# Performance work log

Hardware: AMD Instinct MI355X
Metric: run time of the kernel (lower is better)

## Reference

```python
import jax, jax.numpy as jnp
import numpy as np

B, T, C = 4, 2048, 1024
N_HEAD = 16
HEAD = C // N_HEAD

def setup_inputs() -> dict:
    key = jax.random.key(0)
    ks = jax.random.split(key, 5)
    return {
        "x": jax.random.normal(ks[0], (B, T, C), dtype=jnp.float32),
        "W_attn": jax.random.normal(ks[1], (C, 3 * C), dtype=jnp.float32) * (C ** -0.5),
        "b_attn": jax.random.normal(ks[2], (3 * C,), dtype=jnp.float32) * 0.02,
        "W_proj": jax.random.normal(ks[3], (C, C), dtype=jnp.float32) * (C ** -0.5),
        "b_proj": jax.random.normal(ks[4], (C,), dtype=jnp.float32) * 0.02,
    }

def reference(x, W_attn, b_attn, W_proj, b_proj):
    Bx, Tx, Cx = x.shape
    qkv = x @ W_attn + b_attn  # [B,T,3C]
    q, k, v = jnp.split(qkv, 3, axis=2)
    # [B,T,H,D] -> [B,H,T,D]
    q = q.reshape(Bx, Tx, N_HEAD, HEAD).transpose(0, 2, 1, 3)
    k = k.reshape(Bx, Tx, N_HEAD, HEAD).transpose(0, 2, 1, 3)
    v = v.reshape(Bx, Tx, N_HEAD, HEAD).transpose(0, 2, 1, 3)
    att = jnp.einsum('bhqd,bhkd->bhqk', q, k) * (HEAD ** -0.5)
    causal = jnp.tril(jnp.ones((Tx, Tx), dtype=bool))
    att = jnp.where(causal, att, jnp.float32(-jnp.inf))
    att = jax.nn.softmax(att, axis=-1)
    y = jnp.einsum('bhqk,bhkd->bhqd', att, v)
    y = y.transpose(0, 2, 1, 3).reshape(Bx, Tx, Cx)
    return y @ W_proj + b_proj
```

## Files before the change

kernel.cpp:

```cpp
#include <hip/hip_runtime.h>
#include <stdint.h>

#define NB 4
#define TT 2048
#define CC 1024
#define NH 16
#define DD 64
#define BHH (NB*NH)
#define MROWS (NB*TT)

typedef uint16_t u16;
typedef uint32_t u32;
typedef __bf16 bf16x8 __attribute__((ext_vector_type(8)));
typedef float f32x4 __attribute__((ext_vector_type(4)));
typedef float f32x16 __attribute__((ext_vector_type(16)));

__device__ __forceinline__ u16 f2bf(float f) {
    union { float f; uint32_t u; } v; v.f = f;
    uint32_t u = v.u;
    return (u16)((u + 0x7FFF + ((u >> 16) & 1)) >> 16);
}

__device__ __forceinline__ u32 cvtpk(float lo, float hi) {
    u32 r;
    asm volatile("v_cvt_pk_bf16_f32 %0, %1, %2" : "=v"(r) : "v"(lo), "v"(hi));
    return r;
}

__device__ __forceinline__ void plswap(u32& a, u32& b) {
    asm volatile("v_permlane32_swap_b32 %0, %1" : "+v"(a), "+v"(b));
}

__device__ __forceinline__ bf16x8 mk8(u32 a, u32 b, u32 c, u32 d) {
    union { u32 u[4]; bf16x8 v; } x;
    x.u[0] = a; x.u[1] = b; x.u[2] = c; x.u[3] = d;
    return x.v;
}

__device__ __forceinline__ void gl_lds16(const u16* g, u16* l) {
    __builtin_amdgcn_global_load_lds(
        (const __attribute__((address_space(1))) unsigned int*)g,
        (__attribute__((address_space(3))) unsigned int*)l, 16, 0, 0);
}

__device__ __forceinline__ f32x4 mfma16(bf16x8 a, bf16x8 b, f32x4 c) {
    return __builtin_amdgcn_mfma_f32_16x16x32_bf16(a, b, c, 0, 0, 0);
}
__device__ __forceinline__ f32x16 mfma32(bf16x8 a, bf16x8 b, f32x16 c) {
    return __builtin_amdgcn_mfma_f32_32x32x16_bf16(a, b, c, 0, 0, 0);
}

__global__ __launch_bounds__(256) void k_f2b(const float* __restrict__ in,
                                             u16* __restrict__ out, int n) {
    const int i = (blockIdx.x * 256 + threadIdx.x) * 4;
    if (i >= n) return;
    const float4 v = *(const float4*)(in + i);
    ushort4 o;
    o.x = f2bf(v.x); o.y = f2bf(v.y); o.z = f2bf(v.z); o.w = f2bf(v.w);
    *(ushort4*)(out + i) = o;
}

__global__ __launch_bounds__(256) void k_transpose_cvt(const float* __restrict__ in,
                                                       u16* __restrict__ out,
                                                       int R, int N) {
    __shared__ float t[32][33];
    const int n0 = blockIdx.x * 32, r0 = blockIdx.y * 32;
    const int c  = threadIdx.x & 31, rq = threadIdx.x >> 5;
#pragma unroll
    for (int i = 0; i < 4; ++i) {
        int r = rq + i * 8;
        t[r][c] = in[(r0 + r) * N + n0 + c];
    }
    __syncthreads();
#pragma unroll
    for (int i = 0; i < 4; ++i) {
        int r = rq + i * 8;
        out[(n0 + r) * R + r0 + c] = f2bf(t[c][r]);
    }
}

__device__ __forceinline__ void gemm_tile(const u16* __restrict__ A,
                                          const u16* __restrict__ Bt,
                                          int m0, int n0, f32x4 acc[4][4]) {
    __shared__ __align__(16) u16 As[128 * 32];
    __shared__ __align__(16) u16 Bs[128 * 32];
    const int tid = threadIdx.x;
    const int l = tid & 63, w = tid >> 6;
    const int wr = w >> 1, wc = w & 1;
    const int lr = l & 15, lg = l >> 4;
    const int srow = tid >> 2;
    const int scolh = (tid & 3) << 3;

    const u16* a0 = A + (m0 + srow) * 1024 + scolh;
    const u16* a1 = A + (m0 + 64 + srow) * 1024 + scolh;
    const u16* b0 = Bt + (n0 + srow) * 1024 + scolh;
    const u16* b1 = Bt + (n0 + 64 + srow) * 1024 + scolh;
    u16* as0 = &As[w * 512];
    u16* as1 = &As[2048 + w * 512];
    u16* bs0 = &Bs[w * 512];
    u16* bs1 = &Bs[2048 + w * 512];

    for (int kt = 0; kt < 32; ++kt) {
        const int ko = kt * 32;
        gl_lds16(a0 + ko, as0);
        gl_lds16(a1 + ko, as1);
        gl_lds16(b0 + ko, bs0);
        gl_lds16(b1 + ko, bs1);
        __syncthreads();
        bf16x8 af[4], bfr[4];
#pragma unroll
        for (int m = 0; m < 4; ++m)
            af[m] = *(const bf16x8*)&As[(wr * 64 + m * 16 + lr) * 32 + lg * 8];
#pragma unroll
        for (int n = 0; n < 4; ++n)
            bfr[n] = *(const bf16x8*)&Bs[(wc * 64 + n * 16 + lr) * 32 + lg * 8];
#pragma unroll
        for (int m = 0; m < 4; ++m)
#pragma unroll
            for (int n = 0; n < 4; ++n)
                acc[m][n] = mfma16(af[m], bfr[n], acc[m][n]);
        __syncthreads();
    }
}

__global__ __launch_bounds__(256) void k_gemm_qkv(const u16* __restrict__ X,
                                                  const u16* __restrict__ Wt,
                                                  const float* __restrict__ bias,
                                                  u16* __restrict__ Qo,
                                                  u16* __restrict__ Ko,
                                                  u16* __restrict__ Vto) {
    f32x4 acc[4][4];
#pragma unroll
    for (int m = 0; m < 4; ++m)
#pragma unroll
        for (int n = 0; n < 4; ++n) acc[m][n] = (f32x4){0.f, 0.f, 0.f, 0.f};
    const int n0 = blockIdx.x * 128, m0 = blockIdx.y * 128;
    gemm_tile(X, Wt, m0, n0, acc);

    const int tid = threadIdx.x, l = tid & 63, w = tid >> 6;
    const int wr = w >> 1, wc = w & 1, lr = l & 15, lg = l >> 4;
#pragma unroll
    for (int n = 0; n < 4; ++n) {
        const int c = n0 + wc * 64 + n * 16 + lr;
        const float bv = bias[c];
        const int which = c >> 10, cc = c & 1023, h = cc >> 6, d = cc & 63;
#pragma unroll
        for (int m = 0; m < 4; ++m) {
            const int rbase = m0 + wr * 64 + m * 16 + lg * 4;
#pragma unroll
            for (int j = 0; j < 4; ++j) {
                const int r = rbase + j;
                const int b = r >> 11, t = r & 2047;
                const int bh = b * NH + h;
                const u16 o = f2bf(acc[m][n][j] + bv);
                if (which == 0)      Qo[(bh * TT + t) * DD + d] = o;
                else if (which == 1) Ko[(bh * TT + t) * DD + d] = o;
                else                 Vto[(bh * DD + d) * TT + t] = o;
            }
        }
    }
}

__global__ __launch_bounds__(256) void k_gemm_proj(const u16* __restrict__ Yin,
                                                   const u16* __restrict__ Wt,
                                                   const float* __restrict__ bias,
                                                   float* __restrict__ out) {
    f32x4 acc[4][4];
#pragma unroll
    for (int m = 0; m < 4; ++m)
#pragma unroll
        for (int n = 0; n < 4; ++n) acc[m][n] = (f32x4){0.f, 0.f, 0.f, 0.f};
    const int n0 = blockIdx.x * 128, m0 = blockIdx.y * 128;
    gemm_tile(Yin, Wt, m0, n0, acc);

    const int tid = threadIdx.x, l = tid & 63, w = tid >> 6;
    const int wr = w >> 1, wc = w & 1, lr = l & 15, lg = l >> 4;
#pragma unroll
    for (int n = 0; n < 4; ++n) {
        const int c = n0 + wc * 64 + n * 16 + lr;
        const float bv = bias[c];
#pragma unroll
        for (int m = 0; m < 4; ++m) {
            const int rbase = m0 + wr * 64 + m * 16 + lg * 4;
#pragma unroll
            for (int j = 0; j < 4; ++j) {
                const int r = rbase + j;
                out[r * CC + c] = acc[m][n][j] + bv;
            }
        }
    }
}

__global__ __launch_bounds__(256) void k_attn(const u16* __restrict__ Qg_,
                                              const u16* __restrict__ Kg_,
                                              const u16* __restrict__ Vg_,
                                              u16* __restrict__ Y) {
    __shared__ __align__(16) u16 Ks[2][64 * 64];
    __shared__ __align__(16) u16 Vs[2][64 * 64];

    const int id = blockIdx.x;
    const int qi = 15 - (id >> 6);
    const int bh = id & 63;
    const int q0 = qi * 128;
    const u16* Qg = Qg_ + (size_t)bh * TT * DD;
    const u16* Kg = Kg_ + (size_t)bh * TT * DD;
    const u16* Vg = Vg_ + (size_t)bh * DD * TT;
    const int tid = threadIdx.x, l = tid & 63, w = tid >> 6;
    const int lq = l & 31, hi = l >> 5;
    const int qs = q0 + w * 32;

    unsigned dmask = 0;
#pragma unroll
    for (int r = 0; r < 16; ++r) {
        const int kvloc = (r & 3) + 8 * (r >> 2) + 4 * hi;
        if (kvloc > lq) dmask |= (1u << r);
    }

    const u16* qrow = Qg + (qs + lq) * DD + hi * 8;
    bf16x8 qf0 = *(const bf16x8*)(qrow);
    bf16x8 qf1 = *(const bf16x8*)(qrow + 16);
    bf16x8 qf2 = *(const bf16x8*)(qrow + 32);
    bf16x8 qf3 = *(const bf16x8*)(qrow + 48);

    f32x16 o0 = {}, o1 = {};
    float mrun = -1e30f, lrun = 0.f;
    const float C2 = 0.18033688011112042f;
    const int nt = 2 * qi + 2;

    auto stage = [&](int t, int b) {
        const int kv0 = t * 64;
#pragma unroll
        for (int iss = 0; iss < 2; ++iss) {
            const int s = iss * 4096 + tid * 16;
            const int row = s >> 7;
            const int colb = (s & 127) ^ ((row & 7) << 4);
            const int ldsoff = (iss * 4096 + w * 1024) >> 1;
            gl_lds16(Kg + (kv0 + row) * DD + (colb >> 1), &Ks[b][ldsoff]);
            gl_lds16(Vg + row * TT + kv0 + (colb >> 1),   &Vs[b][ldsoff]);
        }
    };

    stage(0, 0);
    __syncthreads();

    for (int t = 0; t < nt; ++t) {
        const int b = t & 1;
        if (t + 1 < nt) stage(t + 1, b ^ 1);
        const int kv0 = t * 64;

#pragma unroll
        for (int s = 0; s < 2; ++s) {
            const int kvs = kv0 + 32 * s;
            if (kvs > qs) continue;

            f32x16 st = {};
#pragma unroll
            for (int i = 0; i < 4; ++i) {
                const int row = 32 * s + lq;
                const int byte = (32 * i + 16 * hi) ^ ((row & 7) << 4);
                const bf16x8 kf = *(const bf16x8*)&Ks[b][(row * 128 + byte) >> 1];
                if (i == 0) st = mfma32(kf, qf0, st);
                else if (i == 1) st = mfma32(kf, qf1, st);
                else if (i == 2) st = mfma32(kf, qf2, st);
                else st = mfma32(kf, qf3, st);
            }

            if (kvs == qs) {
#pragma unroll
                for (int r = 0; r < 16; ++r)
                    if ((dmask >> r) & 1) st[r] = -1e30f;
            }

            float mx = st[0];
#pragma unroll
            for (int r = 1; r < 16; ++r) mx = fmaxf(mx, st[r]);
            mx = fmaxf(mx, __shfl_xor(mx, 32));

            if (!__all(mx <= mrun)) {
                const float mn = fmaxf(mrun, mx);
                const float scl = __builtin_amdgcn_exp2f((mrun - mn) * C2);
                mrun = mn;
                lrun *= scl;
#pragma unroll
                for (int r = 0; r < 16; ++r) { o0[r] *= scl; o1[r] *= scl; }
            }

            float psum = 0.f;
            u32 pk0, pk1, pk2, pk3, pk4, pk5, pk6, pk7;
            {
                float pa, pb;
                pa = __builtin_amdgcn_exp2f((st[0] - mrun) * C2);
                pb = __builtin_amdgcn_exp2f((st[1] - mrun) * C2);
                psum += pa + pb; pk0 = cvtpk(pa, pb);
                pa = __builtin_amdgcn_exp2f((st[2] - mrun) * C2);
                pb = __builtin_amdgcn_exp2f((st[3] - mrun) * C2);
                psum += pa + pb; pk1 = cvtpk(pa, pb);
                pa = __builtin_amdgcn_exp2f((st[4] - mrun) * C2);
                pb = __builtin_amdgcn_exp2f((st[5] - mrun) * C2);
                psum += pa + pb; pk2 = cvtpk(pa, pb);
                pa = __builtin_amdgcn_exp2f((st[6] - mrun) * C2);
                pb = __builtin_amdgcn_exp2f((st[7] - mrun) * C2);
                psum += pa + pb; pk3 = cvtpk(pa, pb);
                pa = __builtin_amdgcn_exp2f((st[8] - mrun) * C2);
                pb = __builtin_amdgcn_exp2f((st[9] - mrun) * C2);
                psum += pa + pb; pk4 = cvtpk(pa, pb);
                pa = __builtin_amdgcn_exp2f((st[10] - mrun) * C2);
                pb = __builtin_amdgcn_exp2f((st[11] - mrun) * C2);
                psum += pa + pb; pk5 = cvtpk(pa, pb);
                pa = __builtin_amdgcn_exp2f((st[12] - mrun) * C2);
                pb = __builtin_amdgcn_exp2f((st[13] - mrun) * C2);
                psum += pa + pb; pk6 = cvtpk(pa, pb);
                pa = __builtin_amdgcn_exp2f((st[14] - mrun) * C2);
                pb = __builtin_amdgcn_exp2f((st[15] - mrun) * C2);
                psum += pa + pb; pk7 = cvtpk(pa, pb);
            }
            lrun += psum;

            plswap(pk0, pk2); plswap(pk1, pk3);
            plswap(pk4, pk6); plswap(pk5, pk7);
            const bf16x8 pf0 = mk8(pk0, pk1, pk2, pk3);
            const bf16x8 pf1 = mk8(pk4, pk5, pk6, pk7);

#pragma unroll
            for (int dh = 0; dh < 2; ++dh) {
#pragma unroll
                for (int ks = 0; ks < 2; ++ks) {
                    const int row = 32 * dh + lq;
                    const int byte = (64 * s + 32 * ks + 16 * hi) ^ ((row & 7) << 4);
                    const bf16x8 vf = *(const bf16x8*)&Vs[b][(row * 128 + byte) >> 1];
                    if (dh == 0) o0 = mfma32(vf, ks ? pf1 : pf0, o0);
                    else         o1 = mfma32(vf, ks ? pf1 : pf0, o1);
                }
            }
        }
        if (t + 1 < nt) __syncthreads();
    }

    lrun += __shfl_xor(lrun, 32);
    const float inv = 1.0f / lrun;
    const int bb = bh >> 4, h = bh & 15;
    u16* yrow = Y + (size_t)(bb * TT + qs + lq) * CC + h * DD;
#pragma unroll
    for (int rq = 0; rq < 4; ++rq) {
        const int d0 = 8 * rq + 4 * hi;
        const u32 w0 = cvtpk(o0[rq * 4 + 0] * inv, o0[rq * 4 + 1] * inv);
        const u32 w1 = cvtpk(o0[rq * 4 + 2] * inv, o0[rq * 4 + 3] * inv);
        *(uint2*)&yrow[d0] = make_uint2(w0, w1);
        const u32 w2 = cvtpk(o1[rq * 4 + 0] * inv, o1[rq * 4 + 1] * inv);
        const u32 w3 = cvtpk(o1[rq * 4 + 2] * inv, o1[rq * 4 + 3] * inv);
        *(uint2*)&yrow[32 + d0] = make_uint2(w2, w3);
    }
}

extern "C" void kernel_launch(void* const* d_in, const int* in_sizes, int n_in,
                              void* d_out, int out_size, void* d_ws, size_t ws_size,
                              hipStream_t stream) {
    const float* X  = (const float*)d_in[0];
    const float* Wa = (const float*)d_in[1];
    const float* ba = (const float*)d_in[2];
    const float* Wp = (const float*)d_in[3];
    const float* bp = (const float*)d_in[4];
    float* out = (float*)d_out;

    u16* ws  = (u16*)d_ws;
    u16* Xb  = ws;
    u16* WtA = Xb + (size_t)MROWS * CC;
    u16* WtP = WtA + 3072 * 1024;
    u16* Qb  = WtP + 1024 * 1024;
    u16* Kb  = Qb + (size_t)BHH * TT * DD;
    u16* Vtb = Kb + (size_t)BHH * TT * DD;
    u16* Yb  = Vtb + (size_t)BHH * TT * DD;

    k_f2b<<<dim3(MROWS * CC / 1024), 256, 0, stream>>>(X, Xb, MROWS * CC);
    k_transpose_cvt<<<dim3(96, 32), 256, 0, stream>>>(Wa, WtA, 1024, 3072);
    k_transpose_cvt<<<dim3(32, 32), 256, 0, stream>>>(Wp, WtP, 1024, 1024);
    k_gemm_qkv<<<dim3(24, 64), 256, 0, stream>>>(Xb, WtA, ba, Qb, Kb, Vtb);
    k_attn<<<dim3(1024), 256, 0, stream>>>(Qb, Kb, Vtb, Yb);
    k_gemm_proj<<<dim3(8, 64), 256, 0, stream>>>(Yb, WtP, bp, out);
}
```

Measured before the change: 205.5 us.

## Rewrite GEMMs as 256x256 double-buffered pipelined tiles with swizzled LDS

Replaces the 128x128 single-buffered GEMM tile, which synchronised twice per 32-wide K step, with a 256x256 tile over 8 waves. The new tile uses 64-wide K slices, double-buffered LDS with XOR swizzling, and an interleaved schedule of half-tile global-to-LDS loads against MFMA quadrants using barriers, priority hints and explicit waitcnts. The goal is to hide global load latency, cut LDS bank conflicts and raise arithmetic intensity for both the QKV and projection GEMMs. The cost is a much more fragile hand schedule and higher register and LDS use. The proj GEMM now launches only 128 blocks, which may underfill the GPU.

```diff
diff --git a/kernel.cpp b/kernel.cpp
--- a/kernel.cpp
+++ b/kernel.cpp
@@ -79,113 +79,175 @@
     }
 }
 
-__device__ __forceinline__ void gemm_tile(const u16* __restrict__ A,
-                                          const u16* __restrict__ Bt,
-                                          int m0, int n0, f32x4 acc[4][4]) {
-    __shared__ __align__(16) u16 As[128 * 32];
-    __shared__ __align__(16) u16 Bs[128 * 32];
-    const int tid = threadIdx.x;
-    const int l = tid & 63, w = tid >> 6;
-    const int wr = w >> 1, wc = w & 1;
+
+__device__ __forceinline__ bf16x8 ldsf(const u16* t, int row, int c2) {
+    return *(const bf16x8*)&t[(row * 128 + (c2 ^ ((row & 7) << 4))) >> 1];
+}
+
+__device__ __forceinline__ void stage_half(const u16* __restrict__ g, int grow0,
+                                           int kt, u16* lds_tile, int h,
+                                           int tid, int w) {
+#pragma unroll
+    for (int c = 0; c < 2; ++c) {
+        const int dest = h * 16384 + c * 8192 + tid * 16;
+        const int row  = dest >> 7;
+        const int c2   = (dest & 127) ^ ((row & 7) << 4);
+        gl_lds16(g + (size_t)(grow0 + row) * 1024 + kt * 64 + (c2 >> 1),
+                 lds_tile + ((h * 16384 + c * 8192 + w * 1024) >> 1));
+    }
+}
+
+#define BAR() __builtin_amdgcn_s_barrier()
+#define LGKM0() do { asm volatile("s_waitcnt lgkmcnt(0)" ::: "memory"); \
+                     __builtin_amdgcn_sched_barrier(0); } while (0)
+#define SETP(x) __builtin_amdgcn_s_setprio(x)
+
+#define RD_A(DST, BUF, H) \
+    { _Pragma("unroll") for (int mf_ = 0; mf_ < 4; ++mf_) { \
+      _Pragma("unroll") for (int ks_ = 0; ks_ < 2; ++ks_) { \
+        DST[mf_][ks_] = ldsf(BUF, ar0 + (H) * 64 + mf_ * 16 + lr, ks_ * 64 + lg * 16); } } }
+
+#define RD_B(DST, BUF, H) \
+    { _Pragma("unroll") for (int nf_ = 0; nf_ < 2; ++nf_) { \
+      _Pragma("unroll") for (int ks_ = 0; ks_ < 2; ++ks_) { \
+        DST[nf_][ks_] = ldsf(BUF, br0 + (H) * 32 + nf_ * 16 + lr, ks_ * 64 + lg * 16); } } }
+
+#define QUAD(MB, NB, AF, BF) \
+    { _Pragma("unroll") for (int mf_ = 0; mf_ < 4; ++mf_) { \
+      _Pragma("unroll") for (int nf_ = 0; nf_ < 2; ++nf_) { \
+        _Pragma("unroll") for (int ks_ = 0; ks_ < 2; ++ks_) { \
+          acc[(MB) + mf_][(NB) + nf_] = \
+              mfma16(AF[mf_][ks_], BF[nf_][ks_], acc[(MB) + mf_][(NB) + nf_]); } } } }
+
+__device__ __forceinline__ void gemm256(const u16* __restrict__ A,
+                                        const u16* __restrict__ Bt,
+                                        int m0, int n0, f32x4 acc[8][4]) {
+    __shared__ __align__(16) u16 As[2][16384];
+    __shared__ __align__(16) u16 Bs[2][16384];
+    const int tid = threadIdx.x, l = tid & 63, w = tid >> 6;
+    const int wr = w >> 2, wc = w & 3;
     const int lr = l & 15, lg = l >> 4;
-    const int srow = tid >> 2;
-    const int scolh = (tid & 3) << 3;
-
-    const u16* a0 = A + (m0 + srow) * 1024 + scolh;
-    const u16* a1 = A + (m0 + 64 + srow) * 1024 + scolh;
-    const u16* b0 = Bt + (n0 + srow) * 1024 + scolh;
-    const u16* b1 = Bt + (n0 + 64 + srow) * 1024 + scolh;
-    u16* as0 = &As[w * 512];
-    u16* as1 = &As[2048 + w * 512];
-    u16* bs0 = &Bs[w * 512];
-    u16* bs1 = &Bs[2048 + w * 512];
-
-    for (int kt = 0; kt < 32; ++kt) {
-        const int ko = kt * 32;
-        gl_lds16(a0 + ko, as0);
-        gl_lds16(a1 + ko, as1);
-        gl_lds16(b0 + ko, bs0);
-        gl_lds16(b1 + ko, bs1);
-        __syncthreads();
-        bf16x8 af[4], bfr[4];
-#pragma unroll
-        for (int m = 0; m < 4; ++m)
-            af[m] = *(const bf16x8*)&As[(wr * 64 + m * 16 + lr) * 32 + lg * 8];
-#pragma unroll
-        for (int n = 0; n < 4; ++n)
-            bfr[n] = *(const bf16x8*)&Bs[(wc * 64 + n * 16 + lr) * 32 + lg * 8];
-#pragma unroll
-        for (int m = 0; m < 4; ++m)
-#pragma unroll
-            for (int n = 0; n < 4; ++n)
-                acc[m][n] = mfma16(af[m], bfr[n], acc[m][n]);
-        __syncthreads();
-    }
-}
-
-__global__ __launch_bounds__(256) void k_gemm_qkv(const u16* __restrict__ X,
-                                                  const u16* __restrict__ Wt,
-                                                  const float* __restrict__ bias,
-                                                  u16* __restrict__ Qo,
-                                                  u16* __restrict__ Ko,
-                                                  u16* __restrict__ Vto) {
-    f32x4 acc[4][4];
-#pragma unroll
-    for (int m = 0; m < 4; ++m)
+    const int ar0 = wr * 128, br0 = wc * 64;
+
+    stage_half(A,  m0, 0, As[0], 0, tid, w);
+    stage_half(A,  m0, 0, As[0], 1, tid, w);
+    stage_half(Bt, n0, 0, Bs[0], 0, tid, w);
+    stage_half(Bt, n0, 0, Bs[0], 1, tid, w);
+    stage_half(Bt, n0, 1, Bs[1], 0, tid, w);
+    stage_half(Bt, n0, 1, Bs[1], 1, tid, w);
+    asm volatile("s_waitcnt vmcnt(4)" ::: "memory");
+    BAR();
+
+    bf16x8 af[4][2], b0[2][2], b1[2][2];
+
+    for (int t = 0; t < 8; ++t) {
+        const bool last = (t == 7);
+        const int kO = 2 * t + 1, kN = 2 * t + 2, kN1 = 2 * t + 3;
+
+        RD_A(af, As[0], 0);
+        RD_B(b0, Bs[0], 0);
+        stage_half(A, m0, kO, As[1], 0, tid, w);
+        BAR(); LGKM0();
+        SETP(1); QUAD(0, 0, af, b0); SETP(0); BAR();
+        RD_B(b1, Bs[0], 1);
+        stage_half(A, m0, kO, As[1], 1, tid, w);
+        BAR(); LGKM0();
+        SETP(1); QUAD(0, 2, af, b1); SETP(0); BAR();
+        RD_A(af, As[0], 1);
+        if (!last) stage_half(Bt, n0, kN, Bs[0], 0, tid, w);
+        BAR(); LGKM0();
+        SETP(1); QUAD(4, 2, af, b1); SETP(0); BAR();
+        if (!last) stage_half(Bt, n0, kN, Bs[0], 1, tid, w);
+        BAR(); LGKM0();
+        SETP(1); QUAD(4, 0, af, b0); SETP(0);
+        if (last) asm volatile("s_waitcnt vmcnt(0)" ::: "memory");
+        else      asm volatile("s_waitcnt vmcnt(4)" ::: "memory");
+        BAR();
+
+        RD_A(af, As[1], 0);
+        RD_B(b0, Bs[1], 0);
+        if (!last) stage_half(A, m0, kN, As[0], 0, tid, w);
+        BAR(); LGKM0();
+        SETP(1); QUAD(0, 0, af, b0); SETP(0); BAR();
+        RD_B(b1, Bs[1], 1);
+        if (!last) stage_half(A, m0, kN, As[0], 1, tid, w);
+        BAR(); LGKM0();
+        SETP(1); QUAD(0, 2, af, b1); SETP(0); BAR();
+        RD_A(af, As[1], 1);
+        if (!last) stage_half(Bt, n0, kN1, Bs[1], 0, tid, w);
+        BAR(); LGKM0();
+        SETP(1); QUAD(4, 2, af, b1); SETP(0); BAR();
+        if (!last) stage_half(Bt, n0, kN1, Bs[1], 1, tid, w);
+        BAR(); LGKM0();
+        SETP(1); QUAD(4, 0, af, b0); SETP(0);
+        if (!last) asm volatile("s_waitcnt vmcnt(4)" ::: "memory");
+        BAR();
+    }
+}
+
+__global__ __launch_bounds__(512, 2) void k_gemm_qkv(const u16* __restrict__ X,
+                                                     const u16* __restrict__ Wt,
+                                                     const float* __restrict__ bias,
+                                                     u16* __restrict__ Qo,
+                                                     u16* __restrict__ Ko,
+                                                     u16* __restrict__ Vto) {
+    f32x4 acc[8][4];
+#pragma unroll
+    for (int m = 0; m < 8; ++m)
 #pragma unroll
         for (int n = 0; n < 4; ++n) acc[m][n] = (f32x4){0.f, 0.f, 0.f, 0.f};
-    const int n0 = blockIdx.x * 128, m0 = blockIdx.y * 128;
-    gemm_tile(X, Wt, m0, n0, acc);
+    const int n0 = blockIdx.x * 256, m0 = blockIdx.y * 256;
+    gemm256(X, Wt, m0, n0, acc);
 
     const int tid = threadIdx.x, l = tid & 63, w = tid >> 6;
-    const int wr = w >> 1, wc = w & 1, lr = l & 15, lg = l >> 4;
-#pragma unroll
-    for (int n = 0; n < 4; ++n) {
-        const int c = n0 + wc * 64 + n * 16 + lr;
+    const int wr = w >> 2, wc = w & 3, lr = l & 15, lg = l >> 4;
+#pragma unroll
+    for (int nf = 0; nf < 4; ++nf) {
+        const int c = n0 + wc * 64 + nf * 16 + lr;
         const float bv = bias[c];
         const int which = c >> 10, cc = c & 1023, h = cc >> 6, d = cc & 63;
 #pragma unroll
-        for (int m = 0; m < 4; ++m) {
-            const int rbase = m0 + wr * 64 + m * 16 + lg * 4;
+        for (int mf = 0; mf < 8; ++mf) {
+            const int rbase = m0 + wr * 128 + mf * 16 + lg * 4;
 #pragma unroll
             for (int j = 0; j < 4; ++j) {
                 const int r = rbase + j;
-                const int b = r >> 11, t = r & 2047;
+                const int b = r >> 11, tt = r & 2047;
                 const int bh = b * NH + h;
-                const u16 o = f2bf(acc[m][n][j] + bv);
-                if (which == 0)      Qo[(bh * TT + t) * DD + d] = o;
-                else if (which == 1) Ko[(bh * TT + t) * DD + d] = o;
-                else                 Vto[(bh * DD + d) * TT + t] = o;
+                const u16 o = f2bf(acc[mf][nf][j] + bv);
+                if (which == 0)      Qo[(bh * TT + tt) * DD + d] = o;
+                else if (which == 1) Ko[(bh * TT + tt) * DD + d] = o;
+                else                 Vto[(bh * DD + d) * TT + tt] = o;
             }
         }
     }
 }
 
-__global__ __launch_bounds__(256) void k_gemm_proj(const u16* __restrict__ Yin,
-                                                   const u16* __restrict__ Wt,
-                                                   const float* __restrict__ bias,
-                                                   float* __restrict__ out) {
-    f32x4 acc[4][4];
-#pragma unroll
-    for (int m = 0; m < 4; ++m)
+__global__ __launch_bounds__(512, 2) void k_gemm_proj(const u16* __restrict__ Yin,
+                                                      const u16* __restrict__ Wt,
+                                                      const float* __restrict__ bias,
+                                                      float* __restrict__ out) {
+    f32x4 acc[8][4];
+#pragma unroll
+    for (int m = 0; m < 8; ++m)
 #pragma unroll
         for (int n = 0; n < 4; ++n) acc[m][n] = (f32x4){0.f, 0.f, 0.f, 0.f};
-    const int n0 = blockIdx.x * 128, m0 = blockIdx.y * 128;
-    gemm_tile(Yin, Wt, m0, n0, acc);
+    const int n0 = blockIdx.x * 256, m0 = blockIdx.y * 256;
+    gemm256(Yin, Wt, m0, n0, acc);
 
     const int tid = threadIdx.x, l = tid & 63, w = tid >> 6;
-    const int wr = w >> 1, wc = w & 1, lr = l & 15, lg = l >> 4;
-#pragma unroll
-    for (int n = 0; n < 4; ++n) {
-        const int c = n0 + wc * 64 + n * 16 + lr;
+    const int wr = w >> 2, wc = w & 3, lr = l & 15, lg = l >> 4;
+#pragma unroll
+    for (int nf = 0; nf < 4; ++nf) {
+        const int c = n0 + wc * 64 + nf * 16 + lr;
         const float bv = bias[c];
 #pragma unroll
-        for (int m = 0; m < 4; ++m) {
-            const int rbase = m0 + wr * 64 + m * 16 + lg * 4;
+        for (int mf = 0; mf < 8; ++mf) {
+            const int rbase = m0 + wr * 128 + mf * 16 + lg * 4;
 #pragma unroll
             for (int j = 0; j < 4; ++j) {
                 const int r = rbase + j;
-                out[r * CC + c] = acc[m][n][j] + bv;
+                out[r * CC + c] = acc[mf][nf][j] + bv;
             }
         }
     }
@@ -374,7 +436,7 @@
     k_f2b<<<dim3(MROWS * CC / 1024), 256, 0, stream>>>(X, Xb, MROWS * CC);
     k_transpose_cvt<<<dim3(96, 32), 256, 0, stream>>>(Wa, WtA, 1024, 3072);
     k_transpose_cvt<<<dim3(32, 32), 256, 0, stream>>>(Wp, WtP, 1024, 1024);
-    k_gemm_qkv<<<dim3(24, 64), 256, 0, stream>>>(Xb, WtA, ba, Qb, Kb, Vtb);
+    k_gemm_qkv<<<dim3(12, 32), 512, 0, stream>>>(Xb, WtA, ba, Qb, Kb, Vtb);
     k_attn<<<dim3(1024), 256, 0, stream>>>(Qb, Kb, Vtb, Yb);
-    k_gemm_proj<<<dim3(8, 64), 256, 0, stream>>>(Yb, WtP, bp, out);
-}
+    k_gemm_proj<<<dim3(4, 32), 512, 0, stream>>>(Yb, WtP, bp, out);
+}
```

Result: slower. 216.3 us (+5.3%).

## Double-buffer GEMM LDS tiles with swizzle, BK=64, and XCD-aware block mapping

Applied to the files above, without the earlier changes.

Rewrites the shared GEMM mainloop to use a K-tile of 64 with two LDS buffers, so the next tile's global-to-LDS loads are issued while the current tile is consumed. This halves the number of barriers per K step. LDS addresses are XOR-swizzled to avoid bank conflicts on the fragment reads. Both GEMMs switch to a 1D grid that groups M tiles per XCD for L2 reuse and request two blocks per CU. LDS use grows to 64KB per block, which may limit occupancy.

```diff
diff --git a/kernel.cpp b/kernel.cpp
--- a/kernel.cpp
+++ b/kernel.cpp
@@ -79,63 +79,78 @@
     }
 }
 
-__device__ __forceinline__ void gemm_tile(const u16* __restrict__ A,
+__device__ __forceinline__ void gemm128v2(const u16* __restrict__ A,
                                           const u16* __restrict__ Bt,
                                           int m0, int n0, f32x4 acc[4][4]) {
-    __shared__ __align__(16) u16 As[128 * 32];
-    __shared__ __align__(16) u16 Bs[128 * 32];
-    const int tid = threadIdx.x;
-    const int l = tid & 63, w = tid >> 6;
+    __shared__ __align__(16) u16 As[2][128 * 64];
+    __shared__ __align__(16) u16 Bs[2][128 * 64];
+    const int tid = threadIdx.x, l = tid & 63, w = tid >> 6;
     const int wr = w >> 1, wc = w & 1;
     const int lr = l & 15, lg = l >> 4;
-    const int srow = tid >> 2;
-    const int scolh = (tid & 3) << 3;
-
-    const u16* a0 = A + (m0 + srow) * 1024 + scolh;
-    const u16* a1 = A + (m0 + 64 + srow) * 1024 + scolh;
-    const u16* b0 = Bt + (n0 + srow) * 1024 + scolh;
-    const u16* b1 = Bt + (n0 + 64 + srow) * 1024 + scolh;
-    u16* as0 = &As[w * 512];
-    u16* as1 = &As[2048 + w * 512];
-    u16* bs0 = &Bs[w * 512];
-    u16* bs1 = &Bs[2048 + w * 512];
-
-    for (int kt = 0; kt < 32; ++kt) {
-        const int ko = kt * 32;
-        gl_lds16(a0 + ko, as0);
-        gl_lds16(a1 + ko, as1);
-        gl_lds16(b0 + ko, bs0);
-        gl_lds16(b1 + ko, bs1);
+
+    auto stage = [&](int kt, int b) {
+#pragma unroll
+        for (int line = 0; line < 4; ++line) {
+            const int s = line * 4096 + tid * 16;
+            const int row = s >> 7;
+            const int colb = (s & 127) ^ ((row & 7) << 4);
+            const int ldsoff = (line * 4096 + w * 1024) >> 1;
+            gl_lds16(A  + (size_t)(m0 + row) * 1024 + kt * 64 + (colb >> 1),
+                     &As[b][ldsoff]);
+            gl_lds16(Bt + (size_t)(n0 + row) * 1024 + kt * 64 + (colb >> 1),
+                     &Bs[b][ldsoff]);
+        }
+    };
+
+    stage(0, 0);
+    __syncthreads();
+
+    for (int kt = 0; kt < 16; ++kt) {
+        const int b = kt & 1;
+        if (kt < 15) stage(kt + 1, b ^ 1);
+#pragma unroll
+        for (int ks = 0; ks < 2; ++ks) {
+            bf16x8 af[4], bf[4];
+#pragma unroll
+            for (int m = 0; m < 4; ++m) {
+                const int row = wr * 64 + m * 16 + lr;
+                const int byteC = (ks * 64 + lg * 16) ^ ((row & 7) << 4);
+                af[m] = *(const bf16x8*)&As[b][(row * 128 + byteC) >> 1];
+            }
+#pragma unroll
+            for (int n = 0; n < 4; ++n) {
+                const int row = wc * 64 + n * 16 + lr;
+                const int byteC = (ks * 64 + lg * 16) ^ ((row & 7) << 4);
+                bf[n] = *(const bf16x8*)&Bs[b][(row * 128 + byteC) >> 1];
+            }
+#pragma unroll
+            for (int m = 0; m < 4; ++m)
+#pragma unroll
+                for (int n = 0; n < 4; ++n)
+                    acc[m][n] = mfma16(af[m], bf[n], acc[m][n]);
+        }
         __syncthreads();
-        bf16x8 af[4], bfr[4];
-#pragma unroll
-        for (int m = 0; m < 4; ++m)
-            af[m] = *(const bf16x8*)&As[(wr * 64 + m * 16 + lr) * 32 + lg * 8];
-#pragma unroll
-        for (int n = 0; n < 4; ++n)
-            bfr[n] = *(const bf16x8*)&Bs[(wc * 64 + n * 16 + lr) * 32 + lg * 8];
-#pragma unroll
-        for (int m = 0; m < 4; ++m)
-#pragma unroll
-            for (int n = 0; n < 4; ++n)
-                acc[m][n] = mfma16(af[m], bfr[n], acc[m][n]);
-        __syncthreads();
-    }
-}
-
-__global__ __launch_bounds__(256) void k_gemm_qkv(const u16* __restrict__ X,
-                                                  const u16* __restrict__ Wt,
-                                                  const float* __restrict__ bias,
-                                                  u16* __restrict__ Qo,
-                                                  u16* __restrict__ Ko,
-                                                  u16* __restrict__ Vto) {
+    }
+}
+
+__global__ __launch_bounds__(256, 2) void k_gemm_qkv(const u16* __restrict__ X,
+                                                     const u16* __restrict__ Wt,
+                                                     const float* __restrict__ bias,
+                                                     u16* __restrict__ Qo,
+                                                     u16* __restrict__ Ko,
+                                                     u16* __restrict__ Vto) {
+    const int id = blockIdx.x;
+    const int xcd = id & 7, lid = id >> 3;
+    const int lm = lid & 7, ln = lid >> 3;
+    const int m0 = (xcd * 8 + lm) * 128;
+    const int n0 = ln * 128;
+
     f32x4 acc[4][4];
 #pragma unroll
     for (int m = 0; m < 4; ++m)
 #pragma unroll
         for (int n = 0; n < 4; ++n) acc[m][n] = (f32x4){0.f, 0.f, 0.f, 0.f};
-    const int n0 = blockIdx.x * 128, m0 = blockIdx.y * 128;
-    gemm_tile(X, Wt, m0, n0, acc);
+    gemm128v2(X, Wt, m0, n0, acc);
 
     const int tid = threadIdx.x, l = tid & 63, w = tid >> 6;
     const int wr = w >> 1, wc = w & 1, lr = l & 15, lg = l >> 4;
@@ -161,17 +176,22 @@
     }
 }
 
-__global__ __launch_bounds__(256) void k_gemm_proj(const u16* __restrict__ Yin,
-                                                   const u16* __restrict__ Wt,
-                                                   const float* __restrict__ bias,
-                                                   float* __restrict__ out) {
+__global__ __launch_bounds__(256, 2) void k_gemm_proj(const u16* __restrict__ Yin,
+                                                      const u16* __restrict__ Wt,
+                                                      const float* __restrict__ bias,
+                                                      float* __restrict__ out) {
+    const int id = blockIdx.x;
+    const int xcd = id & 7, lid = id >> 3;
+    const int lm = lid & 7, ln = lid >> 3;
+    const int m0 = (xcd * 8 + lm) * 128;
+    const int n0 = ln * 128;
+
     f32x4 acc[4][4];
 #pragma unroll
     for (int m = 0; m < 4; ++m)
 #pragma unroll
         for (int n = 0; n < 4; ++n) acc[m][n] = (f32x4){0.f, 0.f, 0.f, 0.f};
-    const int n0 = blockIdx.x * 128, m0 = blockIdx.y * 128;
-    gemm_tile(Yin, Wt, m0, n0, acc);
+    gemm128v2(Yin, Wt, m0, n0, acc);
 
     const int tid = threadIdx.x, l = tid & 63, w = tid >> 6;
     const int wr = w >> 1, wc = w & 1, lr = l & 15, lg = l >> 4;
@@ -374,7 +394,7 @@
     k_f2b<<<dim3(MROWS * CC / 1024), 256, 0, stream>>>(X, Xb, MROWS * CC);
     k_transpose_cvt<<<dim3(96, 32), 256, 0, stream>>>(Wa, WtA, 1024, 3072);
     k_transpose_cvt<<<dim3(32, 32), 256, 0, stream>>>(Wp, WtP, 1024, 1024);
-    k_gemm_qkv<<<dim3(24, 64), 256, 0, stream>>>(Xb, WtA, ba, Qb, Kb, Vtb);
+    k_gemm_qkv<<<dim3(1536), 256, 0, stream>>>(Xb, WtA, ba, Qb, Kb, Vtb);
     k_attn<<<dim3(1024), 256, 0, stream>>>(Qb, Kb, Vtb, Yb);
-    k_gemm_proj<<<dim3(8, 64), 256, 0, stream>>>(Yb, WtP, bp, out);
-}
+    k_gemm_proj<<<dim3(512), 256, 0, stream>>>(Yb, WtP, bp, out);
+}
```

Result: faster. 188.3 us (-8.4%).
